# Optimization experiments

Measured on AMD Instinct MI355X. Metric: run time of the kernel, lower is better.

The kernel has to match this reference:

```python
import jax, jax.numpy as jnp
import numpy as np
from jax import lax

NUM_LAYERS = 1000
DIM = 10
BATCH = 2_000_000


def setup_inputs() -> dict:
    key = jax.random.key(0)
    kx, kw, kb = jax.random.split(key, 3)
    x = jax.random.normal(kx, (BATCH, DIM), dtype=jnp.float32)
    # torch Linear weight is [out, in]; stack all 1000 layers: [L, out, in]
    # std = 1/sqrt(DIM) keeps activation scale roughly stable across 1000 layers
    Ws = jax.random.normal(kw, (NUM_LAYERS, DIM, DIM), dtype=jnp.float32) * (DIM ** -0.5)
    bs = jax.random.normal(kb, (NUM_LAYERS, DIM), dtype=jnp.float32) * 0.01
    return {"x": x, "Ws": Ws, "bs": bs}


def reference(x, Ws, bs):
    # Sequential of 1000 Linear(10,10): h <- h @ W_l.T + b_l, no activation.
    def step(h, wb):
        W, b = wb  # W: [out, in], b: [out]
        return h @ W.T + b, None
    out, _ = lax.scan(step, x, (Ws, bs))
    return out
```

## Files before the change

### kernel.cpp

```cpp
#include <hip/hip_runtime.h>

#define NUM_LAYERS 1000
#define DIM 10
#define STRIDE 112
#define LPB 16
#define NBLK 63

__device__ inline void compose_one(const float* __restrict__ src,
                                   float* __restrict__ dst,
                                   int c, int lane) {
    const float* F = src + (size_t)(2 * c) * STRIDE;
    const float* G = src + (size_t)(2 * c + 1) * STRIDE;
    float colf[DIM], o[DIM];
    #pragma unroll
    for (int r = 0; r < DIM; ++r) colf[r] = F[lane * DIM + r];
    #pragma unroll
    for (int r = 0; r < DIM; ++r) {
        float acc = (lane == DIM) ? G[100 + r] : 0.f;
        #pragma unroll
        for (int k = 0; k < DIM; ++k)
            acc += G[k * DIM + r] * colf[k];
        o[r] = acc;
    }
    float* D = dst + (size_t)c * STRIDE;
    #pragma unroll
    for (int r = 0; r < DIM; ++r) D[lane * DIM + r] = o[r];
}

__global__ __launch_bounds__(1024) void compose16(const float* __restrict__ Ws,
                                                  const float* __restrict__ bs,
                                                  float* __restrict__ wsout) {
    __shared__ float A[LPB * STRIDE];
    __shared__ float B[(LPB / 2) * STRIDE];
    const int tid = threadIdx.x;
    const int blk = blockIdx.x;

    for (int e = tid; e < LPB * 100; e += 1024) {
        int ll = e / 100, rem = e % 100;
        int r = rem / 10, k = rem % 10;
        int l = blk * LPB + ll;
        float v = (l < NUM_LAYERS) ? Ws[(size_t)l * 100 + rem]
                                   : (r == k ? 1.f : 0.f);
        A[ll * STRIDE + k * DIM + r] = v;
    }
    for (int e = tid; e < LPB * DIM; e += 1024) {
        int ll = e / DIM, r = e % DIM;
        int l = blk * LPB + ll;
        float v = (l < NUM_LAYERS) ? bs[(size_t)l * DIM + r] : 0.f;
        A[ll * STRIDE + 100 + r] = v;
    }

    const int wave = tid >> 6, lane = tid & 63;
    const float* src = A;
    float* dst = B;
    for (int n = LPB / 2; n >= 1; n >>= 1) {
        __syncthreads();
        if (wave < n && lane <= DIM) compose_one(src, dst, wave, lane);
        const float* t = dst; dst = (float*)src; src = t;
    }
    __syncthreads();
    if (tid < 110) wsout[(size_t)blk * STRIDE + tid] = A[tid];
}

__global__ __launch_bounds__(1024) void compose_tree64(const float* __restrict__ wsin,
                                                       float* __restrict__ aff) {
    __shared__ float A[64 * STRIDE];
    __shared__ float B[32 * STRIDE];
    const int tid = threadIdx.x;

    for (int e = tid; e < 64 * STRIDE; e += 1024) {
        int chunk = e / STRIDE, pos = e % STRIDE;
        float v;
        if (pos >= 110)      v = 0.f;
        else if (chunk < NBLK) v = wsin[(size_t)chunk * STRIDE + pos];
        else v = (pos < 100 && (pos / 10 == pos % 10)) ? 1.f : 0.f;
        A[e] = v;
    }

    const int wave = tid >> 6, lane = tid & 63;
    const float* src = A;
    float* dst = B;
    for (int n = 32; n >= 1; n >>= 1) {
        __syncthreads();
        if (lane <= DIM)
            for (int c = wave; c < n; c += 16)
                compose_one(src, dst, c, lane);
        const float* t = dst; dst = (float*)src; src = t;
    }
    __syncthreads();
    if (tid < 110) {
        if (tid < 100) {
            int j = tid / DIM, r = tid % DIM;
            aff[r * DIM + j] = A[tid];
        } else {
            aff[tid] = A[tid];
        }
    }
}

__global__ __launch_bounds__(256) void apply_affine(const float* __restrict__ x,
                                                    const float* __restrict__ aff,
                                                    float* __restrict__ out,
                                                    int npairs) {
    __shared__ float s[112];
    if (threadIdx.x < 112)
        s[threadIdx.x] = (threadIdx.x < 110) ? aff[threadIdx.x] : 0.f;
    __syncthreads();

    const int t = blockIdx.x * blockDim.x + threadIdx.x;
    if (t >= npairs) return;

    const float4* xin = (const float4*)x + (size_t)t * 5;
    float4 v0 = xin[0], v1 = xin[1], v2 = xin[2], v3 = xin[3], v4 = xin[4];
    float xv[20] = {v0.x, v0.y, v0.z, v0.w,  v1.x, v1.y, v1.z, v1.w,
                    v2.x, v2.y, v2.z, v2.w,  v3.x, v3.y, v3.z, v3.w,
                    v4.x, v4.y, v4.z, v4.w};
    float o[20];
    #pragma unroll
    for (int rr = 0; rr < 2; ++rr) {
        #pragma unroll
        for (int j = 0; j < DIM; ++j) {
            float acc = s[100 + j];
            #pragma unroll
            for (int k = 0; k < DIM; ++k)
                acc += s[j * DIM + k] * xv[rr * DIM + k];
            o[rr * DIM + j] = acc;
        }
    }

    float4* op = (float4*)out + (size_t)t * 5;
    op[0] = make_float4(o[0],  o[1],  o[2],  o[3]);
    op[1] = make_float4(o[4],  o[5],  o[6],  o[7]);
    op[2] = make_float4(o[8],  o[9],  o[10], o[11]);
    op[3] = make_float4(o[12], o[13], o[14], o[15]);
    op[4] = make_float4(o[16], o[17], o[18], o[19]);
}

extern "C" void kernel_launch(void* const* d_in, const int* in_sizes, int n_in,
                              void* d_out, int out_size, void* d_ws, size_t ws_size,
                              hipStream_t stream) {
    const float* x  = (const float*)d_in[0];
    const float* Ws = (const float*)d_in[1];
    const float* bs = (const float*)d_in[2];
    float* out = (float*)d_out;

    float* ws_chunks = (float*)d_ws;
    float* ws_aff    = ws_chunks + NBLK * STRIDE;

    const int batch  = in_sizes[0] / DIM;
    const int npairs = batch / 2;

    compose16<<<NBLK, 1024, 0, stream>>>(Ws, bs, ws_chunks);
    compose_tree64<<<1, 1024, 0, stream>>>(ws_chunks, ws_aff);

    const int threads = 256;
    const int blocks  = (npairs + threads - 1) / threads;
    apply_affine<<<blocks, threads, 0, stream>>>(x, ws_aff, out, npairs);
}
```

Baseline: 171.5 us.

## Fuse compose kernels via last-block atomic and widen apply to four rows

The two composition kernels are merged into one launch. The last block to finish, detected with an atomic counter and threadfences, performs the 64-way tree reduction, which removes a kernel launch at the cost of a memset. The apply kernel now handles four rows per thread, reads the affine matrix straight into registers instead of through shared memory, and writes with nontemporal stores. This raises register pressure (100 coefficients plus 40 inputs per thread), which risks spills and lower occupancy on a memory-bound kernel.

```diff
diff --git a/kernel.cpp b/kernel.cpp
--- a/kernel.cpp
+++ b/kernel.cpp
@@ -5,6 +5,8 @@
 #define STRIDE 112
 #define LPB 16
 #define NBLK 63
+
+typedef float floatx4 __attribute__((ext_vector_type(4)));
 
 __device__ inline void compose_one(const float* __restrict__ src,
                                    float* __restrict__ dst,
@@ -27,13 +29,17 @@
     for (int r = 0; r < DIM; ++r) D[lane * DIM + r] = o[r];
 }
 
-__global__ __launch_bounds__(1024) void compose16(const float* __restrict__ Ws,
-                                                  const float* __restrict__ bs,
-                                                  float* __restrict__ wsout) {
-    __shared__ float A[LPB * STRIDE];
-    __shared__ float B[(LPB / 2) * STRIDE];
+__global__ __launch_bounds__(1024) void compose_all(const float* __restrict__ Ws,
+                                                    const float* __restrict__ bs,
+                                                    float* __restrict__ chunks,
+                                                    float* __restrict__ aff,
+                                                    unsigned int* __restrict__ counter) {
+    __shared__ float S[96 * STRIDE];
+    float* A = S;
+    float* B = S + 64 * STRIDE;
     const int tid = threadIdx.x;
     const int blk = blockIdx.x;
+    const int wave = tid >> 6, lane = tid & 63;
 
     for (int e = tid; e < LPB * 100; e += 1024) {
         int ll = e / 100, rem = e % 100;
@@ -46,46 +52,44 @@
     for (int e = tid; e < LPB * DIM; e += 1024) {
         int ll = e / DIM, r = e % DIM;
         int l = blk * LPB + ll;
-        float v = (l < NUM_LAYERS) ? bs[(size_t)l * DIM + r] : 0.f;
-        A[ll * STRIDE + 100 + r] = v;
+        A[ll * STRIDE + 100 + r] = (l < NUM_LAYERS) ? bs[(size_t)l * DIM + r] : 0.f;
     }
-
-    const int wave = tid >> 6, lane = tid & 63;
-    const float* src = A;
-    float* dst = B;
-    for (int n = LPB / 2; n >= 1; n >>= 1) {
-        __syncthreads();
-        if (wave < n && lane <= DIM) compose_one(src, dst, wave, lane);
-        const float* t = dst; dst = (float*)src; src = t;
+    {
+        const float* src = A; float* dst = B;
+        for (int n = LPB / 2; n >= 1; n >>= 1) {
+            __syncthreads();
+            if (wave < n && lane <= DIM) compose_one(src, dst, wave, lane);
+            float* t = dst; dst = (float*)src; src = t;
+        }
     }
     __syncthreads();
-    if (tid < 110) wsout[(size_t)blk * STRIDE + tid] = A[tid];
-}
+    if (tid < 110) chunks[(size_t)blk * STRIDE + tid] = A[tid];
 
-__global__ __launch_bounds__(1024) void compose_tree64(const float* __restrict__ wsin,
-                                                       float* __restrict__ aff) {
-    __shared__ float A[64 * STRIDE];
-    __shared__ float B[32 * STRIDE];
-    const int tid = threadIdx.x;
+    __threadfence();
+    __shared__ unsigned int last;
+    if (tid == 0)
+        last = (atomicAdd(counter, 1u) == NBLK - 1) ? 1u : 0u;
+    __syncthreads();
+    if (!last) return;
+    __threadfence();
 
     for (int e = tid; e < 64 * STRIDE; e += 1024) {
-        int chunk = e / STRIDE, pos = e % STRIDE;
+        int c = e / STRIDE, pos = e % STRIDE;
         float v;
         if (pos >= 110)      v = 0.f;
-        else if (chunk < NBLK) v = wsin[(size_t)chunk * STRIDE + pos];
+        else if (c < NBLK)   v = chunks[(size_t)c * STRIDE + pos];
         else v = (pos < 100 && (pos / 10 == pos % 10)) ? 1.f : 0.f;
         A[e] = v;
     }
-
-    const int wave = tid >> 6, lane = tid & 63;
-    const float* src = A;
-    float* dst = B;
-    for (int n = 32; n >= 1; n >>= 1) {
-        __syncthreads();
-        if (lane <= DIM)
-            for (int c = wave; c < n; c += 16)
-                compose_one(src, dst, c, lane);
-        const float* t = dst; dst = (float*)src; src = t;
+    {
+        const float* src = A; float* dst = B;
+        for (int n = 32; n >= 1; n >>= 1) {
+            __syncthreads();
+            if (lane <= DIM)
+                for (int c = wave; c < n; c += 16)
+                    compose_one(src, dst, c, lane);
+            float* t = dst; dst = (float*)src; src = t;
+        }
     }
     __syncthreads();
     if (tid < 110) {
@@ -101,39 +105,43 @@
 __global__ __launch_bounds__(256) void apply_affine(const float* __restrict__ x,
                                                     const float* __restrict__ aff,
                                                     float* __restrict__ out,
-                                                    int npairs) {
-    __shared__ float s[112];
-    if (threadIdx.x < 112)
-        s[threadIdx.x] = (threadIdx.x < 110) ? aff[threadIdx.x] : 0.f;
-    __syncthreads();
+                                                    int nquads) {
+    int t = blockIdx.x * blockDim.x + threadIdx.x;
+    if (t >= nquads) t = nquads - 1;
 
-    const int t = blockIdx.x * blockDim.x + threadIdx.x;
-    if (t >= npairs) return;
+    const floatx4* xin = (const floatx4*)x + (size_t)t * 10;
+    floatx4 v[10];
+    #pragma unroll
+    for (int i = 0; i < 10; ++i) v[i] = xin[i];
 
-    const float4* xin = (const float4*)x + (size_t)t * 5;
-    float4 v0 = xin[0], v1 = xin[1], v2 = xin[2], v3 = xin[3], v4 = xin[4];
-    float xv[20] = {v0.x, v0.y, v0.z, v0.w,  v1.x, v1.y, v1.z, v1.w,
-                    v2.x, v2.y, v2.z, v2.w,  v3.x, v3.y, v3.z, v3.w,
-                    v4.x, v4.y, v4.z, v4.w};
-    float o[20];
+    float a[100], b[DIM];
     #pragma unroll
-    for (int rr = 0; rr < 2; ++rr) {
+    for (int i = 0; i < 100; ++i) a[i] = aff[i];
+    #pragma unroll
+    for (int j = 0; j < DIM; ++j) b[j] = aff[100 + j];
+
+    __builtin_amdgcn_sched_barrier(0);
+
+    const float* xv = (const float*)v;
+    float o[40];
+    #pragma unroll
+    for (int j = 0; j < DIM; ++j) {
         #pragma unroll
-        for (int j = 0; j < DIM; ++j) {
-            float acc = s[100 + j];
+        for (int rr = 0; rr < 4; ++rr) {
+            float acc = b[j];
             #pragma unroll
             for (int k = 0; k < DIM; ++k)
-                acc += s[j * DIM + k] * xv[rr * DIM + k];
+                acc += a[j * DIM + k] * xv[rr * DIM + k];
             o[rr * DIM + j] = acc;
         }
     }
 
-    float4* op = (float4*)out + (size_t)t * 5;
-    op[0] = make_float4(o[0],  o[1],  o[2],  o[3]);
-    op[1] = make_float4(o[4],  o[5],  o[6],  o[7]);
-    op[2] = make_float4(o[8],  o[9],  o[10], o[11]);
-    op[3] = make_float4(o[12], o[13], o[14], o[15]);
-    op[4] = make_float4(o[16], o[17], o[18], o[19]);
+    floatx4* op = (floatx4*)out + (size_t)t * 10;
+    #pragma unroll
+    for (int i = 0; i < 10; ++i) {
+        floatx4 w = { o[4*i], o[4*i+1], o[4*i+2], o[4*i+3] };
+        __builtin_nontemporal_store(w, op + i);
+    }
 }
 
 extern "C" void kernel_launch(void* const* d_in, const int* in_sizes, int n_in,
@@ -144,16 +152,17 @@
     const float* bs = (const float*)d_in[2];
     float* out = (float*)d_out;
 
-    float* ws_chunks = (float*)d_ws;
-    float* ws_aff    = ws_chunks + NBLK * STRIDE;
+    unsigned int* counter = (unsigned int*)d_ws;
+    float* ws_aff    = (float*)d_ws + 32;
+    float* ws_chunks = (float*)d_ws + 32 + 128;
 
     const int batch  = in_sizes[0] / DIM;
-    const int npairs = batch / 2;
+    const int nquads = batch / 4;
 
-    compose16<<<NBLK, 1024, 0, stream>>>(Ws, bs, ws_chunks);
-    compose_tree64<<<1, 1024, 0, stream>>>(ws_chunks, ws_aff);
+    (void)hipMemsetAsync(counter, 0, sizeof(unsigned int), stream);
+    compose_all<<<NBLK, 1024, 0, stream>>>(Ws, bs, ws_chunks, ws_aff, counter);
 
     const int threads = 256;
-    const int blocks  = (npairs + threads - 1) / threads;
-    apply_affine<<<blocks, threads, 0, stream>>>(x, ws_aff, out, npairs);
+    const int blocks  = (nquads + threads - 1) / threads;
+    apply_affine<<<blocks, threads, 0, stream>>>(x, ws_aff, out, nquads);
 }
```

Result: slower. 301.3 us (+75.7%).
